# Performance work log

Measured on AMD Instinct MI355X. Metric: run time of the kernel, lower is better.

## Reference

```python
import math
import jax, jax.numpy as jnp
import numpy as np

ROUNDS = 4
BUCKET_LEN = 64
NEG_BIG = -1e9
NEG_SELF = -1e5
EPS = 1e-12


def look_back(x):
    # x: [B, n_buckets, bucket_len, ...]; prepend previous bucket (circular) along bucket_len axis
    return jnp.concatenate([jnp.roll(x, 1, axis=1), x], axis=2)


def gather_dim1(x, idx):
    # torch expand_gather: broadcast x and idx to common shape, gather along axis 1
    shape = np.broadcast_shapes(x.shape, idx.shape)
    return jnp.take_along_axis(jnp.broadcast_to(x, shape), jnp.broadcast_to(idx, shape), axis=1)


def setup_inputs() -> dict:
    key = jax.random.key(0)
    k1, k2, k3 = jax.random.split(key, 3)
    B, L, d_k = 16, 4096, 64
    n_buckets = L // BUCKET_LEN
    query = jax.random.normal(k1, (B, L, d_k), dtype=jnp.float32)
    value = jax.random.normal(k2, (B, L, d_k), dtype=jnp.float32)
    rand_matrix = jax.random.normal(k3, (B, d_k, ROUNDS, n_buckets // 2), dtype=jnp.float32)
    return {"query": query, "value": value, "rand_matrix": rand_matrix, "seed": 0}


def lsh_hashes(query, rand_matrix):
    # LocalitySensitiveHash.forward
    B, L, d_k = query.shape
    qn = query / jnp.maximum(jnp.linalg.norm(query, axis=-1, keepdims=True), EPS)
    rm = rand_matrix / jnp.linalg.norm(rand_matrix, axis=1, keepdims=True)
    mm = jnp.einsum('bld,bdrn->blrn', qn, rm)  # [B, L, rounds, n_buckets//2]
    h = jnp.argmax(jnp.concatenate([mm, -mm], axis=-1), axis=-1).astype(jnp.int32)  # [B, L, rounds]
    return h * L + jnp.arange(L, dtype=jnp.int32)[None, :, None]  # unique per position


def _lsh_attention(query, value, rand_matrix):
    B, L, d_k = query.shape
    R, bl = ROUNDS, BUCKET_LEN
    nb = L // bl

    h = lsh_hashes(query, rand_matrix)
    sorted_hashes = jnp.sort(h, axis=1)
    hash_indice = jnp.argsort(h, axis=1)               # [B, L, R]
    original_indice = jnp.argsort(hash_indice, axis=1)  # reverse_sort

    # reorder queries by hash, bucketize: [B, nb, bl, d_k, R]
    rq = gather_dim1(query[:, :, :, None], hash_indice[:, :, None, :]).reshape(B, nb, bl, d_k, R)
    lb_key = look_back(rq)
    lb_key = lb_key / jnp.maximum(jnp.linalg.norm(lb_key, axis=-2, keepdims=True), EPS)
    scores = jnp.einsum('bnidr,bnjdr->bnijr', rq, lb_key) / math.sqrt(d_k)  # [B, nb, bl, 2bl, R]

    # mask: different buckets, causal, self
    sh = sorted_hashes.reshape(B, nb, bl, R) // L  # bucket id
    scores = jnp.where(sh[..., None, :] != look_back(sh)[..., None, :, :], NEG_BIG, scores)
    qi = hash_indice.reshape(B, nb, bl, R).astype(jnp.int32)
    ki = look_back(qi)  # [B, nb, 2bl, R]
    scores = jnp.where(qi[..., None, :] < ki[..., None, :, :], NEG_BIG, scores)
    scores = jnp.where(qi[..., None, :] == ki[..., None, :, :], NEG_SELF, scores)

    # duplicate-key counting across rounds (get_dup_keys)
    ki_full = jnp.broadcast_to(ki[:, :, None, :, :], (B, nb, bl, 2 * bl, R)).reshape(B, L, 2 * bl, R)
    ki_full = gather_dim1(ki_full, original_indice[:, :, None, :])
    flat = ki_full.reshape(B, L, 2 * bl * R)
    s_idx = jnp.argsort(flat, axis=-1)
    s = jnp.take_along_axis(flat, s_idx, axis=-1)
    counts = jnp.ones_like(s)
    for i in range(1, R):
        eq = (s[..., i:] == s[..., :-i]).astype(s.dtype)
        counts = counts + jnp.pad(eq, ((0, 0), (0, 0), (i, 0))) + jnp.pad(eq, ((0, 0), (0, 0), (0, i)))
    inv = jnp.argsort(s_idx, axis=-1)
    count_key = jnp.take_along_axis(counts, inv, axis=-1).reshape(B, L, 2 * bl, R)
    count_key = gather_dim1(count_key, hash_indice[:, :, None, :])

    # duplicate-adjusted softmax
    scores = scores.reshape(B, L, 2 * bl, R)
    lse = jax.nn.logsumexp(scores, axis=2)  # [B, L, R]
    softmax_qk = jnp.exp(scores - jnp.log(count_key.astype(scores.dtype)) - lse[:, :, None, :])

    rv = gather_dim1(value[:, :, :, None], hash_indice[:, :, None, :]).reshape(B, nb, bl, d_k, R)
    sm = softmax_qk.reshape(B, nb, bl, 2 * bl, R)
    attn = jnp.einsum('bnijr,bnjdr->bnidr', sm, look_back(rv)).reshape(B, L, d_k, R)
    attn = gather_dim1(attn, original_indice[:, :, None, :])
    lse = jnp.take_along_axis(lse, original_indice, axis=1)
    round_weights = jax.nn.softmax(lse, axis=1)  # dim=1 (length) exactly as in the source
    return jnp.einsum('bldr,blr->bld', attn, round_weights)


def reference(query, value, rand_matrix, seed):
    # seed is unused by the original forward body; dropout skipped (eval mode)
    return _lsh_attention(query, value, rand_matrix)
```

## Files before the change

kernel.cpp:

```cpp
#include <hip/hip_runtime.h>
#include <math.h>

#define B_  16
#define L_  4096
#define D_  64
#define R_  4
#define NB_ 64
#define BL_ 64

typedef _Float16 f16x8 __attribute__((ext_vector_type(8)));
typedef _Float16 f16x2 __attribute__((ext_vector_type(2)));
typedef float    f32x4 __attribute__((ext_vector_type(4)));


__global__ __launch_bounds__(256, 4) void k_hash(const float* __restrict__ q,
                                                 const float* __restrict__ value,
                                                 const float* __restrict__ rm,
                                                 int* __restrict__ h_ws,
                                                 float* __restrict__ qscale_g,
                                                 _Float16* __restrict__ khf,
                                                 _Float16* __restrict__ vhf) {
    __shared__ __align__(16) char smem[36864];
    _Float16* Rhi = (_Float16*)smem;
    _Float16* Rlo = (_Float16*)(smem + 18432);
    float*    Sc  = (float*)smem;

    int blk = blockIdx.x;
    int b = blk >> 6, chunk = blk & 63;
    int tid = threadIdx.x;
    int w = tid >> 6, lane = tid & 63, quad = lane >> 4, l15 = lane & 15;

    {
        int row = chunk * 64 + (tid >> 2), sub = tid & 3;
        const float4* vp = (const float4*)(value + ((size_t)(b * L_ + row)) * 64 + sub * 16);
        f16x8 h0, h1;
        #pragma unroll
        for (int c = 0; c < 2; c++) {
            float4 t0 = vp[2 * c], t1 = vp[2 * c + 1];
            f16x8& hd = c ? h1 : h0;
            hd[0]=(_Float16)t0.x; hd[1]=(_Float16)t0.y; hd[2]=(_Float16)t0.z; hd[3]=(_Float16)t0.w;
            hd[4]=(_Float16)t1.x; hd[5]=(_Float16)t1.y; hd[6]=(_Float16)t1.z; hd[7]=(_Float16)t1.w;
        }
        _Float16* dst = vhf + ((size_t)(b * L_ + row)) * 64 + sub * 16;
        *(f16x8*)dst = h0;
        *(f16x8*)(dst + 8) = h1;
    }

    {
        int row = tid >> 1, dh2 = (tid & 1) * 32;
        int rr = row >> 5, nn = row & 31;
        const float* rpb = rm + (size_t)b * 8192 + rr * 32 + nn;
        float ss = 0.f;
        #pragma unroll
        for (int g = 0; g < 32; g++) { float v = rpb[(dh2 + g) * 128]; ss += v * v; }
        ss += __shfl_xor(ss, 1);
        float rn = 1.0f / sqrtf(ss);
        #pragma unroll
        for (int gg = 0; gg < 4; gg++) {
            f16x8 hv, lv;
            #pragma unroll
            for (int e = 0; e < 8; e++) {
                float f = rpb[(dh2 + gg * 8 + e) * 128] * rn;
                _Float16 h = (_Float16)f;
                hv[e] = h; lv[e] = (_Float16)(f - (float)h);
            }
            *(f16x8*)&Rhi[row * 72 + dh2 + gg * 8] = hv;
            *(f16x8*)&Rlo[row * 72 + dh2 + gg * 8] = lv;
        }
    }

    int qrow = chunk * 64 + w * 16 + l15;
    const float* qp = q + ((size_t)(b * L_ + qrow)) * 64;
    float qv[16];
    #pragma unroll
    for (int kt = 0; kt < 2; kt++) {
        float4 t0 = *(const float4*)(qp + kt * 32 + quad * 8);
        float4 t1 = *(const float4*)(qp + kt * 32 + quad * 8 + 4);
        qv[8*kt+0]=t0.x; qv[8*kt+1]=t0.y; qv[8*kt+2]=t0.z; qv[8*kt+3]=t0.w;
        qv[8*kt+4]=t1.x; qv[8*kt+5]=t1.y; qv[8*kt+6]=t1.z; qv[8*kt+7]=t1.w;
    }
    f16x8 Ahi[2], Alo[2];
    #pragma unroll
    for (int kt = 0; kt < 2; kt++) {
        #pragma unroll
        for (int j = 0; j < 8; j++) {
            _Float16 hi = (_Float16)qv[8*kt+j];
            Ahi[kt][j] = hi;
            Alo[kt][j] = (_Float16)(qv[8*kt+j] - (float)hi);
        }
    }
    {
        float ss = 0.f;
        #pragma unroll
        for (int j = 0; j < 16; j++) ss += qv[j] * qv[j];
        ss += __shfl_xor(ss, 16);
        ss += __shfl_xor(ss, 32);
        float nr = sqrtf(ss); if (nr < 1e-12f) nr = 1e-12f;
        float kscale = 0.18033688f / nr;
        if (quad == 0) qscale_g[(size_t)b * L_ + qrow] = nr * 5.5451774445f;
        _Float16* kd = khf + ((size_t)(b * L_ + qrow)) * 64;
        #pragma unroll
        for (int kt = 0; kt < 2; kt++) {
            f16x8 hv;
            #pragma unroll
            for (int j = 0; j < 8; j++) hv[j] = (_Float16)(qv[8*kt+j] * kscale);
            *(f16x8*)(kd + kt * 32 + quad * 8) = hv;
        }
    }
    __syncthreads();

    f32x4 acc[8];
    #pragma unroll
    for (int jt = 0; jt < 8; jt++) acc[jt] = (f32x4){0.f, 0.f, 0.f, 0.f};
    #pragma unroll
    for (int jt = 0; jt < 8; jt++) {
        #pragma unroll
        for (int kt = 0; kt < 2; kt++) {
            f16x8 bh = *(const f16x8*)&Rhi[(jt * 16 + l15) * 72 + kt * 32 + quad * 8];
            f16x8 bl = *(const f16x8*)&Rlo[(jt * 16 + l15) * 72 + kt * 32 + quad * 8];
            acc[jt] = __builtin_amdgcn_mfma_f32_16x16x32_f16(Ahi[kt], bh, acc[jt], 0, 0, 0);
            acc[jt] = __builtin_amdgcn_mfma_f32_16x16x32_f16(Ahi[kt], bl, acc[jt], 0, 0, 0);
            acc[jt] = __builtin_amdgcn_mfma_f32_16x16x32_f16(Alo[kt], bh, acc[jt], 0, 0, 0);
        }
    }
    __syncthreads();

    #pragma unroll
    for (int jt = 0; jt < 8; jt++) {
        #pragma unroll
        for (int reg = 0; reg < 4; reg++)
            Sc[(w * 16 + quad * 4 + reg) * 133 + jt * 16 + l15] = acc[jt][reg];
    }
    __syncthreads();

    {
        int row = tid & 63, r = tid >> 6;
        const float* sp = &Sc[row * 133 + r * 32];
        float v1 = -1e30f, v2 = -1e30f; int i1 = 0;
        #pragma unroll
        for (int n = 0; n < 32; n++) {
            float v = sp[n];
            float a = fabsf(v);
            int cand = n | ((__float_as_uint(v) >> 26) & 32);
            if (a > v1) i1 = cand;
            v2 = __builtin_amdgcn_fmed3f(a, v1, v2);
            v1 = fmaxf(a, v1);
        }
        int l = chunk * 64 + row;
        if (v1 - v2 < 4e-5f) i1 |= (1 << 30);
        h_ws[((size_t)(b * 4 + r)) * L_ + l] = i1;
    }
}

__global__ __launch_bounds__(256) void k_sort(const int* __restrict__ h_ws,
                                              const float* __restrict__ q,
                                              const float* __restrict__ rm,
                                              int2* __restrict__ metaA,
                                              unsigned char* __restrict__ packB) {
    __shared__ __align__(16) unsigned short cnt[64 * 257];
    __shared__ __align__(16) unsigned short oi_s[256 * 17];
    __shared__ __align__(16) unsigned short p_s[4096];
    __shared__ __align__(16) unsigned short sb_s[4096];
    __shared__ int part[256];
    __shared__ int bstart_s[64];
    __shared__ int flcnt;

    int br = blockIdx.x;
    int b = br >> 2, r = br & 3;
    int t = threadIdx.x;
    const int* hp = h_ws + (size_t)br * L_;

    if (t == 0) flcnt = 0;

    int key[16]; unsigned fmask = 0;
    const int4* hp4 = (const int4*)(hp + t * 16);
    #pragma unroll
    for (int g = 0; g < 4; g++) {
        int4 v = hp4[g];
        int raw[4] = { v.x, v.y, v.z, v.w };
        #pragma unroll
        for (int j = 0; j < 4; j++) {
            int k = g * 4 + j;
            key[k] = raw[j] & 63;
            if (raw[j] & (1 << 30)) fmask |= 1u << k;
        }
    }
    __syncthreads();

    if (fmask) {
        #pragma unroll
        for (int k = 0; k < 16; k++)
            if (fmask & (1u << k)) {
                int slot = atomicAdd(&flcnt, 1);
                sb_s[slot] = (unsigned short)(t * 16 + k);
            }
    }
    __syncthreads();

    {
        int wid = t >> 6, lane = t & 63;
        int fc = flcnt;
        for (int e = wid; e < fc; e += 4) {
            int l = sb_s[e];
            int n = lane & 31;
            const float* rpb = rm + (size_t)b * 8192 + r * 32 + n;
            const float* qr = q + ((size_t)(b * L_ + l)) * 64;
            double s2 = 0.0, dot = 0.0;
            for (int d = 0; d < 64; d++) {
                double m = (double)rpb[d * 128];
                s2 += m * m;
                dot += (double)qr[d] * m;
            }
            double acc = dot / sqrt(s2);
            double v = (lane < 32) ? acc : -acc;
            int idx = lane;
            #pragma unroll
            for (int off = 1; off < 64; off <<= 1) {
                double ov = __shfl_xor(v, off);
                int   oidx = __shfl_xor(idx, off);
                if (ov > v || (ov == v && oidx < idx)) { v = ov; idx = oidx; }
            }
            if (lane == 0) p_s[l] = (unsigned short)idx;
        }
    }
    __syncthreads();
    if (fmask) {
        #pragma unroll
        for (int k = 0; k < 16; k++)
            if (fmask & (1u << k)) key[k] = p_s[t * 16 + k];
    }

    unsigned int* cz = (unsigned int*)cnt;
    #pragma unroll
    for (int i = 0; i < 33; i++) {
        int idx = i * 256 + t;
        if (idx < 8224) cz[idx] = 0;
    }
    __syncthreads();

    #pragma unroll
    for (int k = 0; k < 16; k++) {
        unsigned short* c = &cnt[key[k] * 257 + t];
        *c = (unsigned short)(*c + 1);
    }
    __syncthreads();

    int u = t & 63, s = t >> 6;
    {
        int run = 0;
        int base_idx = u * 257 + s * 64;
        #pragma unroll 16
        for (int i = 0; i < 64; i++) {
            int c = cnt[base_idx + i];
            cnt[base_idx + i] = (unsigned short)run;
            run += c;
        }
        part[s * 64 + u] = run;
    }
    __syncthreads();

    if (t < 64) {
        int p0 = part[t], p1 = part[64 + t], p2 = part[128 + t], p3 = part[192 + t];
        int tot = p0 + p1 + p2 + p3;
        int v = tot;
        #pragma unroll
        for (int off = 1; off < 64; off <<= 1) {
            int o = __shfl_up(v, off);
            if (t >= off) v += o;
        }
        int base = v - tot;
        bstart_s[t] = base;
        part[t]       = base;
        part[64 + t]  = base + p0;
        part[128 + t] = base + p0 + p1;
        part[192 + t] = base + p0 + p1 + p2;
    }
    __syncthreads();

    int sbase = s * 64;
    #pragma unroll
    for (int k = 0; k < 16; k++) {
        int uk = key[k];
        unsigned short* c = &cnt[uk * 257 + t];
        int pos = part[sbase + uk] + *c;
        *c = (unsigned short)(*c + 1);
        int idx = t * 16 + k;
        oi_s[(idx >> 4) * 17 + (idx & 15)] = (unsigned short)pos;
        p_s[pos]  = (unsigned short)idx;
        sb_s[pos] = (unsigned short)bstart_s[uk];
    }
    __syncthreads();

    int2* mp = metaA + (size_t)br * L_;
    unsigned char* pb = packB + ((size_t)b * L_) * 4 + r;
    #pragma unroll
    for (int k = 0; k < 16; k++) {
        int e = k * 256 + t;
        mp[e] = make_int2((int)sb_s[e], (int)p_s[e]);
        int pos = (int)oi_s[(e >> 4) * 17 + (e & 15)];
        pb[(size_t)e * 4] = (unsigned char)(pos >> 6);
    }
}

__global__ __launch_bounds__(256, 4) void k_attn(const float* __restrict__ qscale_g,
                                                 const _Float16* __restrict__ khf,
                                                 const _Float16* __restrict__ vhf,
                                                 const int2* __restrict__ metaA,
                                                 const unsigned int* __restrict__ packA,
                                                 float* __restrict__ lse_ws,
                                                 _Float16* __restrict__ attn_ws) {
    __shared__ _Float16 Ksh[128 * 72];
    __shared__ _Float16 Vt[64 * 136];
    __shared__ int4 kmeta[128];

    int xcd = blockIdx.x & 7, slot = blockIdx.x >> 3;
    int b = xcd * 2 + (slot >> 8);
    int rem = slot & 255, n = rem >> 2, r = rem & 3;
    int tid = threadIdx.x;
    int w = tid >> 6, lane = tid & 63, quad = lane >> 4, l15 = lane & 15;
    int hibase = (b * 4 + r) * L_;
    const int2* mpA = metaA + hibase;
    int nprev = (n + 63) & 63;

    {
        int j = tid >> 1, dh = (tid & 1) * 32;
        int spos = (j < 64) ? (nprev * 64 + j) : (n * 64 + (j - 64));
        int2 ma = mpA[spos];
        const _Float16* src = khf + ((size_t)(b * L_ + ma.y)) * 64 + dh;
        f16x8 t0 = *(const f16x8*)(src);
        f16x8 t1 = *(const f16x8*)(src + 8);
        f16x8 t2 = *(const f16x8*)(src + 16);
        f16x8 t3 = *(const f16x8*)(src + 24);
        if (dh == 0) {
            unsigned int pk = packA[b * L_ + ma.y];
            unsigned int pm1 = ((pk | 0x40404040u) - 0x01010101u) & 0x3f3f3f3fu;
            kmeta[j] = make_int4(ma.x, ma.y, (int)pk, (int)pm1);
        }
        *(f16x8*)&Ksh[j * 72 + dh + 0]  = t0;
        *(f16x8*)&Ksh[j * 72 + dh + 8]  = t1;
        *(f16x8*)&Ksh[j * 72 + dh + 16] = t2;
        *(f16x8*)&Ksh[j * 72 + dh + 24] = t3;
    }
    __syncthreads();

    {
        int m = tid >> 2, sub = tid & 3;
        int y0 = kmeta[2 * m].y, y1 = kmeta[2 * m + 1].y;
        const _Float16* v0 = vhf + ((size_t)(b * L_ + y0)) * 64 + sub * 16;
        const _Float16* v1 = vhf + ((size_t)(b * L_ + y1)) * 64 + sub * 16;
        f16x8 a00 = *(const f16x8*)v0, a01 = *(const f16x8*)(v0 + 8);
        f16x8 a10 = *(const f16x8*)v1, a11 = *(const f16x8*)(v1 + 8);
        #pragma unroll
        for (int d = 0; d < 8; d++) {
            f16x2 hv = { a00[d], a10[d] };
            *(f16x2*)&Vt[(sub * 16 + d) * 136 + 2 * m] = hv;
            f16x2 hw = { a01[d], a11[d] };
            *(f16x2*)&Vt[(sub * 16 + 8 + d) * 136 + 2 * m] = hw;
        }
    }

    f16x8 afr[2];
    afr[0] = *(const f16x8*)&Ksh[(64 + w * 16 + l15) * 72 + quad * 8];
    afr[1] = *(const f16x8*)&Ksh[(64 + w * 16 + l15) * 72 + 32 + quad * 8];

    int4 qm4[4]; int km4z[8]; float qs4[4];
    #pragma unroll
    for (int reg = 0; reg < 4; reg++) {
        qm4[reg] = kmeta[64 + w * 16 + quad * 4 + reg];
        qs4[reg] = qscale_g[(size_t)b * L_ + qm4[reg].y];
    }
    #pragma unroll
    for (int jt = 0; jt < 8; jt++) km4z[jt] = kmeta[jt * 16 + l15].z;

    f32x4 acc[8];
    #pragma unroll
    for (int jt = 0; jt < 8; jt++) acc[jt] = (f32x4){0.f, 0.f, 0.f, 0.f};
    __builtin_amdgcn_s_setprio(1);
    #pragma unroll
    for (int jt = 0; jt < 8; jt++) {
        #pragma unroll
        for (int kt = 0; kt < 2; kt++) {
            f16x8 bfr = *(const f16x8*)&Ksh[(jt * 16 + l15) * 72 + kt * 32 + quad * 8];
            acc[jt] = __builtin_amdgcn_mfma_f32_16x16x32_f16(afr[kt], bfr, acc[jt], 0, 0, 0);
        }
    }
    __builtin_amdgcn_s_setprio(0);
    __syncthreads();

    _Float16* Ph = Ksh;
    float lse_r[4], inv_r[4];
    #pragma unroll
    for (int reg = 0; reg < 4; reg++) {
        int lo = qm4[reg].x - (n - 1) * 64;
        int width = w * 16 + quad * 4 + reg + 64 - lo;
        int jl = l15 - lo;
        float qs = qs4[reg];
        float s[8];
        #pragma unroll
        for (int jt = 0; jt < 8; jt++) {
            float v = acc[jt][reg] * qs;
            int ju = jt * 16 + jl;
            v = ((unsigned)ju < (unsigned)width) ? v : -1.4426951e9f;
            if (ju == width) v = -144269.50f;
            s[jt] = v;
        }
        float m = s[0];
        #pragma unroll
        for (int jt = 1; jt < 8; jt++) m = fmaxf(m, s[jt]);
        #pragma unroll
        for (int off = 1; off < 16; off <<= 1) m = fmaxf(m, __shfl_xor(m, off));
        float te[8], sum = 0.f;
        #pragma unroll
        for (int jt = 0; jt < 8; jt++) { te[jt] = __builtin_amdgcn_exp2f(s[jt] - m); sum += te[jt]; }
        #pragma unroll
        for (int off = 1; off < 16; off <<= 1) sum += __shfl_xor(sum, off);
        inv_r[reg] = __builtin_amdgcn_rcpf(sum);
        lse_r[reg] = m * 0.6931472f + __logf(sum);
        int i = w * 16 + quad * 4 + reg;
        #pragma unroll
        for (int jt = 0; jt < 8; jt++) {
            int z1 = km4z[jt] ^ qm4[reg].z;
            int z2 = km4z[jt] ^ qm4[reg].w;
            int nz = __popc((z1 + 0x7f7f7f7f) & 0x80808080)
                   + __popc((z2 + 0x7f7f7f7f) & 0x80808080);
            float p = te[jt] * __builtin_amdgcn_rcpf((float)(8 - nz));
            Ph[i * 136 + jt * 16 + l15] = (_Float16)p;
        }
    }
    if (l15 == 0) {
        #pragma unroll
        for (int reg = 0; reg < 4; reg++)
            lse_ws[hibase + qm4[reg].y] = lse_r[reg];
    }
    __syncthreads();

    f32x4 oacc[4];
    #pragma unroll
    for (int nt = 0; nt < 4; nt++) oacc[nt] = (f32x4){0.f, 0.f, 0.f, 0.f};
    __builtin_amdgcn_s_setprio(1);
    #pragma unroll
    for (int kt = 0; kt < 4; kt++) {
        f16x8 pa = *(const f16x8*)&Ph[(w * 16 + l15) * 136 + kt * 32 + quad * 8];
        #pragma unroll
        for (int nt = 0; nt < 4; nt++) {
            f16x8 vb = *(const f16x8*)&Vt[(nt * 16 + l15) * 136 + kt * 32 + quad * 8];
            oacc[nt] = __builtin_amdgcn_mfma_f32_16x16x32_f16(pa, vb, oacc[nt], 0, 0, 0);
        }
    }
    __builtin_amdgcn_s_setprio(0);
    __syncthreads();

    _Float16* Pout = Ksh;
    #pragma unroll
    for (int nt = 0; nt < 4; nt++) {
        #pragma unroll
        for (int reg = 0; reg < 4; reg++) {
            int i = w * 16 + quad * 4 + reg;
            Pout[i * 72 + nt * 16 + l15] = (_Float16)(oacc[nt][reg] * inv_r[reg]);
        }
    }
    __syncthreads();

    {
        int row = tid >> 2, part = tid & 3;
        int y = kmeta[64 + row].y;
        _Float16* dst = attn_ws + ((size_t)hibase + y) * 64;
        f16x8 v0 = *(const f16x8*)&Pout[row * 72 + part * 8];
        f16x8 v1 = *(const f16x8*)&Pout[row * 72 + 32 + part * 8];
        *(f16x8*)(dst + part * 8) = v0;
        *(f16x8*)(dst + 32 + part * 8) = v1;
    }
}

__global__ __launch_bounds__(256) void k_rw(const float* __restrict__ lse_ws,
                                            float* __restrict__ rwmax,
                                            float* __restrict__ rwsum) {
    __shared__ float  red[256];
    __shared__ double redd[256];
    int br = blockIdx.x;
    const float* lp = lse_ws + (size_t)br * L_;
    int t = threadIdx.x;
    float m = -1e30f;
    for (int k = t; k < L_; k += 256) m = fmaxf(m, lp[k]);
    red[t] = m; __syncthreads();
    for (int s2 = 128; s2 > 0; s2 >>= 1) {
        if (t < s2) red[t] = fmaxf(red[t], red[t + s2]);
        __syncthreads();
    }
    float mm = red[0];
    double s = 0.0;
    for (int k = t; k < L_; k += 256) s += (double)expf(lp[k] - mm);
    redd[t] = s; __syncthreads();
    for (int s2 = 128; s2 > 0; s2 >>= 1) {
        if (t < s2) redd[t] += redd[t + s2];
        __syncthreads();
    }
    if (t == 0) { rwmax[br] = mm; rwsum[br] = (float)redd[0]; }
}

__global__ __launch_bounds__(256) void k_out(const _Float16* __restrict__ attn_ws,
                                             const float* __restrict__ lse_ws,
                                             const float* __restrict__ rwmax,
                                             const float* __restrict__ rwsum,
                                             float* __restrict__ out) {
    int gid = blockIdx.x * 256 + threadIdx.x;
    int g = gid & 7;
    size_t row = (size_t)(gid >> 3);
    int b = (int)(row >> 12), l = (int)(row & 4095);
    float o[8];
    #pragma unroll
    for (int k = 0; k < 8; k++) o[k] = 0.f;
    #pragma unroll
    for (int r = 0; r < 4; r++) {
        int br = b * 4 + r;
        float wgt = __expf(lse_ws[(size_t)br * L_ + l] - rwmax[br])
                  * __builtin_amdgcn_rcpf(rwsum[br]);
        f16x8 av = *(const f16x8*)&attn_ws[(((size_t)br * L_ + l) << 6) + g * 8];
        #pragma unroll
        for (int k = 0; k < 8; k++) o[k] += (float)av[k] * wgt;
    }
    float4* op = (float4*)(out + row * 64 + g * 8);
    op[0] = make_float4(o[0], o[1], o[2], o[3]);
    op[1] = make_float4(o[4], o[5], o[6], o[7]);
}

extern "C" void kernel_launch(void* const* d_in, const int* in_sizes, int n_in,
                              void* d_out, int out_size, void* d_ws, size_t ws_size,
                              hipStream_t stream) {
    const float* query = (const float*)d_in[0];
    const float* value = (const float*)d_in[1];
    const float* rm    = (const float*)d_in[2];
    char* ws = (char*)d_ws;
    int*       h_ws   = (int*)(ws + ((size_t)1 << 20));
    float*     lse_ws = (float*)(ws + ((size_t)4 << 20));
    float*     rwmax  = (float*)(ws + ((size_t)5 << 20));
    float*     rwsum  = (float*)(ws + ((size_t)5 << 20) + 256);
    _Float16*  attn_ws= (_Float16*)(ws + ((size_t)6 << 20));
    int2*      metaA  = (int2*)(ws + ((size_t)41 << 20));
    unsigned char* packB = (unsigned char*)(ws + ((size_t)43 << 20));
    float*     qscale = (float*)(ws + ((size_t)45 << 20));
    _Float16*  khf    = (_Float16*)(ws + ((size_t)53 << 20));
    _Float16*  vhf    = (_Float16*)(ws + ((size_t)61 << 20));
    float*     out    = (float*)d_out;

    hipLaunchKernelGGL(k_hash,   dim3(1024), dim3(256), 0, stream, query, value, rm,
                       h_ws, qscale, khf, vhf);
    hipLaunchKernelGGL(k_sort,   dim3(64),   dim3(256), 0, stream, h_ws, query, rm,
                       metaA, packB);
    hipLaunchKernelGGL(k_attn,   dim3(4096), dim3(256), 0, stream,
                       qscale, khf, vhf, metaA, (const unsigned int*)packB, lse_ws, attn_ws);
    hipLaunchKernelGGL(k_rw,     dim3(64),   dim3(256), 0, stream, lse_ws, rwmax, rwsum);
    hipLaunchKernelGGL(k_out,    dim3(2048), dim3(256), 0, stream,
                       attn_ws, lse_ws, rwmax, rwsum, out);
}
```

Before: 156.0 us.

## Split attention block across 8 waves with key-half partitioning and cross-wave softmax

Doubles k_attn's block to 512 threads, splitting each query tile's 128 keys between two waves. Row max and row sum are now combined across wave pairs through shared memory, and the PV product splits the output columns the same way. The aim is more parallelism per block and fewer registers per wave, to hide latency better. In exchange it adds two extra block barriers and some shared-memory traffic, and the launch_bounds of (512, 8) may constrain registers.

```diff
diff --git a/kernel.cpp b/kernel.cpp
--- a/kernel.cpp
+++ b/kernel.cpp
@@ -302,7 +302,7 @@
     }
 }
 
-__global__ __launch_bounds__(256, 4) void k_attn(const float* __restrict__ qscale_g,
+__global__ __launch_bounds__(512, 8) void k_attn(const float* __restrict__ qscale_g,
                                                  const _Float16* __restrict__ khf,
                                                  const _Float16* __restrict__ vhf,
                                                  const int2* __restrict__ metaA,
@@ -312,138 +312,152 @@
     __shared__ _Float16 Ksh[128 * 72];
     __shared__ _Float16 Vt[64 * 136];
     __shared__ int4 kmeta[128];
+    __shared__ float Pmax[64 * 2];
+    __shared__ float Psum[64 * 2];
 
     int xcd = blockIdx.x & 7, slot = blockIdx.x >> 3;
     int b = xcd * 2 + (slot >> 8);
     int rem = slot & 255, n = rem >> 2, r = rem & 3;
     int tid = threadIdx.x;
-    int w = tid >> 6, lane = tid & 63, quad = lane >> 4, l15 = lane & 15;
+    int wv = tid >> 6;
+    int wq = wv & 3, wk = wv >> 2;
+    int lane = tid & 63, quad = lane >> 4, l15 = lane & 15;
     int hibase = (b * 4 + r) * L_;
     const int2* mpA = metaA + hibase;
     int nprev = (n + 63) & 63;
 
     {
-        int j = tid >> 1, dh = (tid & 1) * 32;
+        int j = tid >> 2, dh = (tid & 3) * 16;
         int spos = (j < 64) ? (nprev * 64 + j) : (n * 64 + (j - 64));
         int2 ma = mpA[spos];
         const _Float16* src = khf + ((size_t)(b * L_ + ma.y)) * 64 + dh;
         f16x8 t0 = *(const f16x8*)(src);
         f16x8 t1 = *(const f16x8*)(src + 8);
-        f16x8 t2 = *(const f16x8*)(src + 16);
-        f16x8 t3 = *(const f16x8*)(src + 24);
-        if (dh == 0) {
+        if ((tid & 3) == 0) {
             unsigned int pk = packA[b * L_ + ma.y];
             unsigned int pm1 = ((pk | 0x40404040u) - 0x01010101u) & 0x3f3f3f3fu;
             kmeta[j] = make_int4(ma.x, ma.y, (int)pk, (int)pm1);
         }
-        *(f16x8*)&Ksh[j * 72 + dh + 0]  = t0;
-        *(f16x8*)&Ksh[j * 72 + dh + 8]  = t1;
-        *(f16x8*)&Ksh[j * 72 + dh + 16] = t2;
-        *(f16x8*)&Ksh[j * 72 + dh + 24] = t3;
-    }
-    __syncthreads();
-
-    {
-        int m = tid >> 2, sub = tid & 3;
+        *(f16x8*)&Ksh[j * 72 + dh]     = t0;
+        *(f16x8*)&Ksh[j * 72 + dh + 8] = t1;
+    }
+    __syncthreads();
+
+    {
+        int m = tid >> 3, sub = tid & 7;
         int y0 = kmeta[2 * m].y, y1 = kmeta[2 * m + 1].y;
-        const _Float16* v0 = vhf + ((size_t)(b * L_ + y0)) * 64 + sub * 16;
-        const _Float16* v1 = vhf + ((size_t)(b * L_ + y1)) * 64 + sub * 16;
-        f16x8 a00 = *(const f16x8*)v0, a01 = *(const f16x8*)(v0 + 8);
-        f16x8 a10 = *(const f16x8*)v1, a11 = *(const f16x8*)(v1 + 8);
+        const _Float16* v0 = vhf + ((size_t)(b * L_ + y0)) * 64 + sub * 8;
+        const _Float16* v1 = vhf + ((size_t)(b * L_ + y1)) * 64 + sub * 8;
+        f16x8 a0 = *(const f16x8*)v0;
+        f16x8 a1 = *(const f16x8*)v1;
         #pragma unroll
         for (int d = 0; d < 8; d++) {
-            f16x2 hv = { a00[d], a10[d] };
-            *(f16x2*)&Vt[(sub * 16 + d) * 136 + 2 * m] = hv;
-            f16x2 hw = { a01[d], a11[d] };
-            *(f16x2*)&Vt[(sub * 16 + 8 + d) * 136 + 2 * m] = hw;
+            f16x2 hv = { a0[d], a1[d] };
+            *(f16x2*)&Vt[(sub * 8 + d) * 136 + 2 * m] = hv;
         }
     }
 
     f16x8 afr[2];
-    afr[0] = *(const f16x8*)&Ksh[(64 + w * 16 + l15) * 72 + quad * 8];
-    afr[1] = *(const f16x8*)&Ksh[(64 + w * 16 + l15) * 72 + 32 + quad * 8];
-
-    int4 qm4[4]; int km4z[8]; float qs4[4];
+    afr[0] = *(const f16x8*)&Ksh[(64 + wq * 16 + l15) * 72 + quad * 8];
+    afr[1] = *(const f16x8*)&Ksh[(64 + wq * 16 + l15) * 72 + 32 + quad * 8];
+
+    int lo4[4]; float qs4[4]; int km4z[4];
     #pragma unroll
     for (int reg = 0; reg < 4; reg++) {
-        qm4[reg] = kmeta[64 + w * 16 + quad * 4 + reg];
-        qs4[reg] = qscale_g[(size_t)b * L_ + qm4[reg].y];
-    }
-    #pragma unroll
-    for (int jt = 0; jt < 8; jt++) km4z[jt] = kmeta[jt * 16 + l15].z;
-
-    f32x4 acc[8];
-    #pragma unroll
-    for (int jt = 0; jt < 8; jt++) acc[jt] = (f32x4){0.f, 0.f, 0.f, 0.f};
+        int4 km = kmeta[64 + wq * 16 + quad * 4 + reg];
+        lo4[reg] = km.x - (n - 1) * 64;
+        qs4[reg] = qscale_g[(size_t)b * L_ + km.y];
+    }
+    #pragma unroll
+    for (int jt = 0; jt < 4; jt++) km4z[jt] = kmeta[wk * 64 + jt * 16 + l15].z;
+
+    f32x4 acc[4];
+    #pragma unroll
+    for (int jt = 0; jt < 4; jt++) acc[jt] = (f32x4){0.f, 0.f, 0.f, 0.f};
     __builtin_amdgcn_s_setprio(1);
     #pragma unroll
-    for (int jt = 0; jt < 8; jt++) {
+    for (int jt = 0; jt < 4; jt++) {
         #pragma unroll
         for (int kt = 0; kt < 2; kt++) {
-            f16x8 bfr = *(const f16x8*)&Ksh[(jt * 16 + l15) * 72 + kt * 32 + quad * 8];
+            f16x8 bfr = *(const f16x8*)&Ksh[(wk * 64 + jt * 16 + l15) * 72 + kt * 32 + quad * 8];
             acc[jt] = __builtin_amdgcn_mfma_f32_16x16x32_f16(afr[kt], bfr, acc[jt], 0, 0, 0);
         }
     }
     __builtin_amdgcn_s_setprio(0);
-    __syncthreads();
-
-    _Float16* Ph = Ksh;
-    float lse_r[4], inv_r[4];
+
+    float s[16];
     #pragma unroll
     for (int reg = 0; reg < 4; reg++) {
-        int lo = qm4[reg].x - (n - 1) * 64;
-        int width = w * 16 + quad * 4 + reg + 64 - lo;
-        int jl = l15 - lo;
+        int lo = lo4[reg];
+        int width = wq * 16 + quad * 4 + reg + 64 - lo;
+        int jl = wk * 64 + l15 - lo;
         float qs = qs4[reg];
-        float s[8];
-        #pragma unroll
-        for (int jt = 0; jt < 8; jt++) {
+        #pragma unroll
+        for (int jt = 0; jt < 4; jt++) {
             float v = acc[jt][reg] * qs;
             int ju = jt * 16 + jl;
             v = ((unsigned)ju < (unsigned)width) ? v : -1.4426951e9f;
             if (ju == width) v = -144269.50f;
-            s[jt] = v;
-        }
-        float m = s[0];
-        #pragma unroll
-        for (int jt = 1; jt < 8; jt++) m = fmaxf(m, s[jt]);
+            s[reg * 4 + jt] = v;
+        }
+        float m = fmaxf(fmaxf(s[reg*4], s[reg*4+1]), fmaxf(s[reg*4+2], s[reg*4+3]));
         #pragma unroll
         for (int off = 1; off < 16; off <<= 1) m = fmaxf(m, __shfl_xor(m, off));
-        float te[8], sum = 0.f;
-        #pragma unroll
-        for (int jt = 0; jt < 8; jt++) { te[jt] = __builtin_amdgcn_exp2f(s[jt] - m); sum += te[jt]; }
+        if (l15 == 0) Pmax[(wq * 16 + quad * 4 + reg) * 2 + wk] = m;
+    }
+    __syncthreads();
+
+    #pragma unroll
+    for (int reg = 0; reg < 4; reg++) {
+        int i = wq * 16 + quad * 4 + reg;
+        float m = fmaxf(Pmax[i * 2], Pmax[i * 2 + 1]);
+        float sum = 0.f;
+        #pragma unroll
+        for (int jt = 0; jt < 4; jt++) {
+            float te = __builtin_amdgcn_exp2f(s[reg * 4 + jt] - m);
+            s[reg * 4 + jt] = te;
+            sum += te;
+        }
         #pragma unroll
         for (int off = 1; off < 16; off <<= 1) sum += __shfl_xor(sum, off);
+        if (l15 == 0) Psum[i * 2 + wk] = sum;
+    }
+    __syncthreads();
+
+    _Float16* Ph = Ksh;
+    float inv_r[4];
+    #pragma unroll
+    for (int reg = 0; reg < 4; reg++) {
+        int i = wq * 16 + quad * 4 + reg;
+        float sum = Psum[i * 2] + Psum[i * 2 + 1];
         inv_r[reg] = __builtin_amdgcn_rcpf(sum);
-        lse_r[reg] = m * 0.6931472f + __logf(sum);
-        int i = w * 16 + quad * 4 + reg;
-        #pragma unroll
-        for (int jt = 0; jt < 8; jt++) {
-            int z1 = km4z[jt] ^ qm4[reg].z;
-            int z2 = km4z[jt] ^ qm4[reg].w;
+        int4 km = kmeta[64 + wq * 16 + quad * 4 + reg];
+        if (l15 == 0 && wk == 0) {
+            float m = fmaxf(Pmax[i * 2], Pmax[i * 2 + 1]);
+            lse_ws[hibase + km.y] = m * 0.6931472f + __logf(sum);
+        }
+        #pragma unroll
+        for (int jt = 0; jt < 4; jt++) {
+            int z1 = km4z[jt] ^ km.z;
+            int z2 = km4z[jt] ^ km.w;
             int nz = __popc((z1 + 0x7f7f7f7f) & 0x80808080)
                    + __popc((z2 + 0x7f7f7f7f) & 0x80808080);
-            float p = te[jt] * __builtin_amdgcn_rcpf((float)(8 - nz));
-            Ph[i * 136 + jt * 16 + l15] = (_Float16)p;
-        }
-    }
-    if (l15 == 0) {
-        #pragma unroll
-        for (int reg = 0; reg < 4; reg++)
-            lse_ws[hibase + qm4[reg].y] = lse_r[reg];
-    }
-    __syncthreads();
-
-    f32x4 oacc[4];
-    #pragma unroll
-    for (int nt = 0; nt < 4; nt++) oacc[nt] = (f32x4){0.f, 0.f, 0.f, 0.f};
+            float p = s[reg * 4 + jt] * __builtin_amdgcn_rcpf((float)(8 - nz));
+            Ph[i * 136 + wk * 64 + jt * 16 + l15] = (_Float16)p;
+        }
+    }
+    __syncthreads();
+
+    f32x4 oacc[2];
+    oacc[0] = (f32x4){0.f, 0.f, 0.f, 0.f};
+    oacc[1] = (f32x4){0.f, 0.f, 0.f, 0.f};
     __builtin_amdgcn_s_setprio(1);
     #pragma unroll
     for (int kt = 0; kt < 4; kt++) {
-        f16x8 pa = *(const f16x8*)&Ph[(w * 16 + l15) * 136 + kt * 32 + quad * 8];
-        #pragma unroll
-        for (int nt = 0; nt < 4; nt++) {
-            f16x8 vb = *(const f16x8*)&Vt[(nt * 16 + l15) * 136 + kt * 32 + quad * 8];
+        f16x8 pa = *(const f16x8*)&Ph[(wq * 16 + l15) * 136 + kt * 32 + quad * 8];
+        #pragma unroll
+        for (int nt = 0; nt < 2; nt++) {
+            f16x8 vb = *(const f16x8*)&Vt[(wk * 32 + nt * 16 + l15) * 136 + kt * 32 + quad * 8];
             oacc[nt] = __builtin_amdgcn_mfma_f32_16x16x32_f16(pa, vb, oacc[nt], 0, 0, 0);
         }
     }
@@ -452,23 +466,20 @@
 
     _Float16* Pout = Ksh;
     #pragma unroll
-    for (int nt = 0; nt < 4; nt++) {
+    for (int nt = 0; nt < 2; nt++) {
         #pragma unroll
         for (int reg = 0; reg < 4; reg++) {
-            int i = w * 16 + quad * 4 + reg;
-            Pout[i * 72 + nt * 16 + l15] = (_Float16)(oacc[nt][reg] * inv_r[reg]);
-        }
-    }
-    __syncthreads();
-
-    {
-        int row = tid >> 2, part = tid & 3;
+            int i = wq * 16 + quad * 4 + reg;
+            Pout[i * 72 + wk * 32 + nt * 16 + l15] = (_Float16)(oacc[nt][reg] * inv_r[reg]);
+        }
+    }
+    __syncthreads();
+
+    {
+        int row = tid >> 3, part = tid & 7;
         int y = kmeta[64 + row].y;
         _Float16* dst = attn_ws + ((size_t)hibase + y) * 64;
-        f16x8 v0 = *(const f16x8*)&Pout[row * 72 + part * 8];
-        f16x8 v1 = *(const f16x8*)&Pout[row * 72 + 32 + part * 8];
-        *(f16x8*)(dst + part * 8) = v0;
-        *(f16x8*)(dst + 32 + part * 8) = v1;
+        *(f16x8*)(dst + part * 8) = *(const f16x8*)&Pout[row * 72 + part * 8];
     }
 }
 
@@ -547,7 +558,7 @@
                        h_ws, qscale, khf, vhf);
     hipLaunchKernelGGL(k_sort,   dim3(64),   dim3(256), 0, stream, h_ws, query, rm,
                        metaA, packB);
-    hipLaunchKernelGGL(k_attn,   dim3(4096), dim3(256), 0, stream,
+    hipLaunchKernelGGL(k_attn,   dim3(4096), dim3(512), 0, stream,
                        qscale, khf, vhf, metaA, (const unsigned int*)packB, lse_ws, attn_ws);
     hipLaunchKernelGGL(k_rw,     dim3(64),   dim3(256), 0, stream, lse_ws, rwmax, rwsum);
     hipLaunchKernelGGL(k_out,    dim3(2048), dim3(256), 0, stream,
```

New measurement: 169.3 us. 8.5% more time.
